# Optimization experiments

Measured on AMD Instinct MI355X. Metric: run time of the kernel, lower is better.

Reference implementation:

```python
import jax, jax.numpy as jnp
import numpy as np

D_MODEL = 1024
D_FF = 4 * D_MODEL
N = D_MODEL * D_FF          # 4,194,304 == 2**22, so pad_n == N (no padding)
PAD_N = N
FFT_LEN = PAD_N // 2 + 1    # 2,097,153 rfft bins
KEEP = int(FFT_LEN * 0.25)  # 524,288 kept coefficients ('medium')
B, S = 4, 2048


def _decompress(cr, ci, idx, shape, scale):
    # scatter top-k complex coeffs into full rfft spectrum, inverse rfft,
    # reshape to weight matrix and rescale (riemann_decompress)
    coeffs = jax.lax.complex(cr, ci)                      # complex64 [KEEP]
    full = jnp.zeros((FFT_LEN,), jnp.complex64).at[idx].set(coeffs)
    w = jnp.fft.irfft(full, n=PAD_N)                      # [PAD_N] real
    return w.reshape(shape) * scale                       # scale is [1], broadcasts


def setup_inputs() -> dict:
    key = jax.random.key(0)
    ks = jax.random.split(key, 9)
    return {
        "x": jax.random.normal(ks[0], (B, S, D_MODEL), jnp.float32),
        "c_fc_coeffs_real": jax.random.normal(ks[1], (KEEP,), jnp.float32),
        "c_fc_coeffs_imag": jax.random.normal(ks[2], (KEEP,), jnp.float32),
        "c_fc_indices": jnp.arange(KEEP, dtype=jnp.int32),
        "c_fc_scale": jax.random.uniform(ks[3], (1,), jnp.float32, 0.5, 1.5),
        "c_fc_bias": jax.random.normal(ks[4], (D_FF,), jnp.float32),
        "c_proj_coeffs_real": jax.random.normal(ks[5], (KEEP,), jnp.float32),
        "c_proj_coeffs_imag": jax.random.normal(ks[6], (KEEP,), jnp.float32),
        "c_proj_indices": jnp.arange(KEEP, dtype=jnp.int32),
        "c_proj_scale": jax.random.uniform(ks[7], (1,), jnp.float32, 0.5, 1.5),
        "c_proj_bias": jax.random.normal(ks[8], (D_MODEL,), jnp.float32),
    }


def reference(x, c_fc_coeffs_real, c_fc_coeffs_imag, c_fc_indices, c_fc_scale,
              c_fc_bias, c_proj_coeffs_real, c_proj_coeffs_imag, c_proj_indices,
              c_proj_scale, c_proj_bias):
    # c_fc.weight stored [d_model, d_ff]; F.linear(x, W.T) == x @ W
    w_fc = _decompress(c_fc_coeffs_real, c_fc_coeffs_imag, c_fc_indices,
                       (D_MODEL, D_FF), c_fc_scale)
    h = jnp.einsum('bsd,df->bsf', x, w_fc) + c_fc_bias
    h = jax.nn.gelu(h, approximate=False)  # nn.GELU() exact erf form
    w_proj = _decompress(c_proj_coeffs_real, c_proj_coeffs_imag, c_proj_indices,
                         (D_FF, D_MODEL), c_proj_scale)
    return jnp.einsum('bsf,fd->bsd', h, w_proj) + c_proj_bias
```

## Files before the change

### kernel.cpp

```cpp
#include <hip/hip_runtime.h>
#include <hip/hip_bf16.h>
#include <hip/hip_fp8.h>
#include <math.h>

#define M_HALF 2097152
#define W_SCALE 256.0f

typedef __bf16 bf16_t;
typedef unsigned char u8;
typedef __attribute__((ext_vector_type(4))) float f32x4;

#define GLOBAL_AS __attribute__((address_space(1)))
#define LDS_AS    __attribute__((address_space(3)))

__device__ __forceinline__ u8 to_fp8(float v) {
    __hip_fp8_e4m3 t(v);
    return *reinterpret_cast<u8*>(&t);
}

__device__ __forceinline__ float2 cadd(float2 a, float2 b){ return make_float2(a.x+b.x, a.y+b.y); }
__device__ __forceinline__ float2 csub(float2 a, float2 b){ return make_float2(a.x-b.x, a.y-b.y); }
__device__ __forceinline__ float2 cmul(float2 a, float2 b){ return make_float2(a.x*b.x-a.y*b.y, a.x*b.y+a.y*b.x); }
__device__ __forceinline__ float2 cmuli(float2 a){ return make_float2(-a.y, a.x); }

__device__ __forceinline__ void radix8_inv(const float2 v[8], float2 X[8]) {
    const float cc = 0.70710678118654752f;
    float2 a0 = cadd(v[0], v[4]), a1 = cadd(v[1], v[5]), a2 = cadd(v[2], v[6]), a3 = cadd(v[3], v[7]);
    float2 b0 = csub(v[0], v[4]), b1 = csub(v[1], v[5]), b2 = csub(v[2], v[6]), b3 = csub(v[3], v[7]);
    b1 = cmul(b1, make_float2(cc, cc));
    b2 = cmuli(b2);
    b3 = cmul(b3, make_float2(-cc, cc));
    float2 c0 = cadd(a0, a2), c1 = cadd(a1, a3), d0 = csub(a0, a2), d1 = cmuli(csub(a1, a3));
    float2 e0 = cadd(b0, b2), e1 = cadd(b1, b3), f0 = csub(b0, b2), f1 = cmuli(csub(b1, b3));
    X[0] = cadd(c0, c1); X[4] = csub(c0, c1); X[2] = cadd(d0, d1); X[6] = csub(d0, d1);
    X[1] = cadd(e0, e1); X[5] = csub(e0, e1); X[3] = cadd(f0, f1); X[7] = csub(f0, f1);
}


__global__ __launch_bounds__(256) void zero2_kernel(float2* p, int n) {
    int i = blockIdx.x*256 + threadIdx.x;
    if (i < n) p[i] = make_float2(0.f, 0.f);
}

__global__ __launch_bounds__(256) void scatter2_kernel(const float* __restrict__ crA,
                                                       const float* __restrict__ ciA,
                                                       const int* __restrict__ idxA,
                                                       const float* __restrict__ crB,
                                                       const float* __restrict__ ciB,
                                                       const int* __restrict__ idxB,
                                                       float2* __restrict__ specA,
                                                       float2* __restrict__ specB, int keep) {
    int i = blockIdx.x*256 + threadIdx.x;
    if (i < keep) {
        int k = idxA[i];
        long pos = (k < M_HALF) ? ((long)(k & 511)*4096 + (k >> 9)) : (long)M_HALF;
        specA[pos] = make_float2(crA[i], ciA[i]);
    } else if (i < 2*keep) {
        int t = i - keep;
        int k = idxB[t];
        long pos = (k < M_HALF) ? ((long)(k & 511)*4096 + (k >> 9)) : (long)M_HALF;
        specB[pos] = make_float2(crB[t], ciB[t]);
    }
}


__global__ __launch_bounds__(512) void ifft_p4096_dual(const float2* __restrict__ specTA,
                                                       const float2* __restrict__ specTB,
                                                       float2* __restrict__ dstA,
                                                       float2* __restrict__ dstB,
                                                       const float* __restrict__ scaleA,
                                                       const float* __restrict__ scaleB) {
    __shared__ float2 L[8*656];
    int bb = blockIdx.x;
    const float2* spec; float2* dst; const float* scale;
    if (bb < 512) { spec = specTA; dst = dstA; scale = scaleA; }
    else          { bb -= 512; spec = specTB; dst = dstB; scale = scaleB; }
    const int j = bb;
    const int x = threadIdx.x;
    const float s = scale[0] * (1.0f/(float)M_HALF);
    float2 v[8];
    {
        float ang0 = (float)(3.14159265358979323846 * (double)(j + 512*x) / 2097152.0);
        float sn, cs; sincosf(ang0, &sn, &cs);
        const float2 step = make_float2(0.98078528040323044913f,
                                        0.19509032201612826785f);
        float2 tw = make_float2(cs, sn);
        const long arow = (long)j * 4096;
        const long brow = (long)(512 - j) * 4096;
#pragma unroll
        for (int u = 0; u < 8; ++u) {
            int t = x + 512*u;
            float2 a = spec[arow + t];
            float2 b;
            if (j == 0) b = (t == 0) ? spec[(long)M_HALF] : spec[4096 - t];
            else        b = spec[brow + 4095 - t];
            if (j == 0 && t == 0) { a.y = 0.0f; b.y = 0.0f; }
            float Er = 0.5f*(a.x + b.x), Ei = 0.5f*(a.y - b.y);
            float Tr = 0.5f*(a.x - b.x), Ti = 0.5f*(a.y + b.y);
            float Or = Tr*tw.x - Ti*tw.y, Oi = Tr*tw.y + Ti*tw.x;
            v[u] = make_float2((Er - Oi)*s, (Ei + Or)*s);
            tw = cmul(tw, step);
        }
    }
    float2 E[8];
    radix8_inv(v, E);
    {
        float cb, sb; sincosf((float)x * 0.0015339807878856412f, &sb, &cb);
        float2 wb = make_float2(cb, sb), w = make_float2(1.f, 0.f);
#pragma unroll
        for (int a = 0; a < 8; ++a) { L[a*656 + x] = cmul(E[a], w); w = cmul(w, wb); }
    }
    __syncthreads();
    const int g = x >> 6, xin = x & 63;
    float2* Lg = L + g*656;
    float2 v2[8];
#pragma unroll
    for (int u2 = 0; u2 < 8; ++u2) v2[u2] = Lg[xin + 64*u2];
    float2 E2[8];
    radix8_inv(v2, E2);
    __syncthreads();
    {
        float cb, sb; sincosf((float)xin * 0.012271846303085130f, &sb, &cb);
        float2 wb = make_float2(cb, sb), w = make_float2(1.f, 0.f);
#pragma unroll
        for (int s8 = 0; s8 < 8; ++s8) { Lg[s8*65 + xin] = cmul(E2[s8], w); w = cmul(w, wb); }
    }
    __syncthreads();
    const int p = xin >> 3, xa = xin & 7;
    float2 g2[8];
#pragma unroll
    for (int xb = 0; xb < 8; ++xb) g2[xb] = Lg[p*65 + xa + 8*xb];
    float2 H2[8];
    radix8_inv(g2, H2);
    __syncthreads();
    {
        float cb, sb; sincosf((float)xa * 0.098174770424681039f, &sb, &cb);
        float2 wb = make_float2(cb, sb), w = make_float2(1.f, 0.f);
#pragma unroll
        for (int o8 = 0; o8 < 8; ++o8) { Lg[p*81 + o8*9 + xa] = cmul(H2[o8], w); w = cmul(w, wb); }
    }
    __syncthreads();
    const int pp = xin & 7, sp = xin >> 3;
    float2 r2[8];
#pragma unroll
    for (int xa2 = 0; xa2 < 8; ++xa2) r2[xa2] = Lg[pp*81 + sp*9 + xa2];
    float2 D[8];
    radix8_inv(r2, D);
    __syncthreads();
#pragma unroll
    for (int ob = 0; ob < 8; ++ob) {
        int sg = g + 8*xin + 512*ob;
        L[sg ^ ((sg >> 4) & 7)] = D[ob];
    }
    __syncthreads();
    const long obase = (long)j * 4096;
#pragma unroll
    for (int e = 0; e < 8; ++e) {
        int idx = x + 512*e;
        dst[obase + idx] = L[idx ^ ((idx >> 4) & 7)];
    }
}


__global__ __launch_bounds__(512) void ifft_p512f8_dual(const float2* __restrict__ srcA,
                                                        u8* __restrict__ dstwA,
                                                        const float2* __restrict__ srcB,
                                                        u8* __restrict__ dstwB) {
    __shared__ float2 ex[8 * 642];
    int bb = blockIdx.x;
    const float2* src; u8* dstw;
    if (bb < 512) { src = srcA; dstw = dstwA; }
    else          { bb -= 512; src = srcB; dstw = dstwB; }
    const int tid = threadIdx.x;
    const int jl = tid & 7, x = tid >> 3;
    const int jg = bb * 8 + jl;
    float2* W = ex + jl * 642;
    float2 v[8];
    {
        float a0 = (float)(6.283185307179586 * (double)jg * (double)x / 2097152.0);
        float sn0, cs0; sincosf(a0, &sn0, &cs0);
        float as = (float)(6.283185307179586 * (double)jg / 32768.0);
        float sns, css; sincosf(as, &sns, &css);
        float2 tw = make_float2(cs0, sn0), stepw = make_float2(css, sns);
#pragma unroll
        for (int u = 0; u < 8; ++u) {
            v[u] = cmul(src[jg + (long)(x + 64*u) * 4096], tw);
            tw = cmul(tw, stepw);
        }
    }
    float2 E[8];
    radix8_inv(v, E);
    {
        float cb, sb; sincosf((float)x * 0.012271846303085130f, &sb, &cb);
        float2 wb = make_float2(cb, sb), w = make_float2(1.f, 0.f);
#pragma unroll
        for (int s8 = 0; s8 < 8; ++s8) {
            W[s8*65 + x] = cmul(E[s8], w);
            w = cmul(w, wb);
        }
    }
    __syncthreads();
    const int p = x >> 3, xa = x & 7;
    float2 g[8];
#pragma unroll
    for (int xb = 0; xb < 8; ++xb) g[xb] = W[p*65 + xa + 8*xb];
    float2 H[8];
    radix8_inv(g, H);
    __syncthreads();
    {
        float cb, sb; sincosf((float)xa * 0.098174770424681039f, &sb, &cb);
        float2 wb = make_float2(cb, sb), w = make_float2(1.f, 0.f);
#pragma unroll
        for (int o8 = 0; o8 < 8; ++o8) {
            W[p*81 + o8*9 + xa] = cmul(H[o8], w);
            w = cmul(w, wb);
        }
    }
    __syncthreads();
    const int pp = x & 7, sp = x >> 3;
    float2 r[8];
#pragma unroll
    for (int xa2 = 0; xa2 < 8; ++xa2) r[xa2] = W[pp*81 + sp*9 + xa2];
    float2 Y[8];
    radix8_inv(r, Y);
#pragma unroll
    for (int ob = 0; ob < 8; ++ob) {
        long n = jg + (long)(x + 64*ob) * 4096;
        unsigned short pk = (unsigned short)to_fp8(Y[ob].x * W_SCALE) |
                            ((unsigned short)to_fp8(Y[ob].y * W_SCALE) << 8);
        ((unsigned short*)dstw)[n] = pk;
    }
}


__global__ __launch_bounds__(256) void transpose_f8_dual(const u8* __restrict__ wA,
                                                         u8* __restrict__ wTA,
                                                         const u8* __restrict__ wB,
                                                         u8* __restrict__ wTB) {
    __shared__ u8 tile[32][36];
    int b = blockIdx.x;
    const u8* w; u8* wT; int R, C, bx, by;
    if (b < 4096) { w = wA; wT = wTA; R = 1024; C = 4096; bx = b & 127; by = b >> 7; }
    else { b -= 4096; w = wB; wT = wTB; R = 4096; C = 1024; bx = b & 31; by = b >> 5; }
    int tx = threadIdx.x & 31, ty = threadIdx.x >> 5;
    long c0 = (long)bx * 32, r0 = (long)by * 32;
#pragma unroll
    for (int i = 0; i < 4; ++i)
        tile[ty + i*8][tx] = w[(r0 + ty + i*8) * C + c0 + tx];
    __syncthreads();
#pragma unroll
    for (int i = 0; i < 4; ++i) {
        int c = ty + i*8;
        wT[(c0 + c) * R + r0 + tx] = tile[tx][c];
    }
}


__global__ __launch_bounds__(256) void cvt_fp8_kernel(const float* __restrict__ in,
                                                      u8* __restrict__ out, int n4) {
    int i = blockIdx.x*256 + threadIdx.x;
    if (i < n4) {
        float4 v = ((const float4*)in)[i];
        unsigned int pk = (unsigned int)to_fp8(v.x) |
                          ((unsigned int)to_fp8(v.y) << 8) |
                          ((unsigned int)to_fp8(v.z) << 16) |
                          ((unsigned int)to_fp8(v.w) << 24);
        ((unsigned int*)out)[i] = pk;
    }
}


template<int NITER>
__device__ __forceinline__ void stage_b(const u8* g, int ldB, int row0, int col0B,
                                        u8* lds, int tid) {
    int w = tid >> 6, l = tid & 63;
    int r8 = l >> 3;
    int cg = ((l & 7) ^ r8) << 4;
#pragma unroll
    for (int i = 0; i < NITER; ++i) {
        int chunk = (i << 3) + w;
        const u8* ga = g + (long)(row0 + chunk*8 + r8) * ldB + col0B + cg;
        u8* la = lds + (chunk << 10);
        __builtin_amdgcn_global_load_lds((const GLOBAL_AS unsigned int*)ga,
                                         (LDS_AS unsigned int*)la, 16, 0, 0);
    }
}


template<int EPI>
__global__ __launch_bounds__(512, 6) void gemm_f8(const u8* __restrict__ A,
                                                  const u8* __restrict__ Bt,
                                                  const float* __restrict__ bias,
                                                  void* __restrict__ Cout,
                                                  int M, int N, int K,
                                                  int CR, int CC, int GXC) {
    __shared__ __align__(16) u8 lA[128*128];
    __shared__ __align__(16) u8 lB[128*128];
    const int tid = threadIdx.x;
    const int l = tid & 63, w = tid >> 6;
    const int wr = w >> 2, wc = w & 3;
    int flat = blockIdx.y * gridDim.x + blockIdx.x;
    int r = flat & 7, q = flat >> 3;
    int ty = (r / GXC) * CR + q / CC;
    int tx = (r % GXC) * CC + q % CC;
    const int row0 = ty * 128, col0 = tx * 128;
    const int lr = l & 15, lq = l >> 4;
    const int xr = (lr & 7) << 4;
    f32x4 acc[4][2] = {};
    for (int k0 = 0; k0 < K; k0 += 128) {
        stage_b<2>(A,  K, row0, k0, lA, tid);
        stage_b<2>(Bt, K, col0, k0, lB, tid);
        __syncthreads();
#pragma unroll
        for (int kk = 0; kk < 4; ++kk) {
            long af[4], bfr[2];
            const int kb = (kk*32 + lq*8) ^ xr;
#pragma unroll
            for (int mi = 0; mi < 4; ++mi)
                af[mi] = *(const long*)(lA + (wr*64 + mi*16 + lr)*128 + kb);
#pragma unroll
            for (int ni = 0; ni < 2; ++ni)
                bfr[ni] = *(const long*)(lB + (wc*32 + ni*16 + lr)*128 + kb);
#pragma unroll
            for (int mi = 0; mi < 4; ++mi)
#pragma unroll
                for (int ni = 0; ni < 2; ++ni)
                    acc[mi][ni] = __builtin_amdgcn_mfma_f32_16x16x32_fp8_fp8(
                        af[mi], bfr[ni], acc[mi][ni], 0, 0, 0);
        }
        __syncthreads();
    }
    const float inv_s = 1.0f / W_SCALE;
#pragma unroll
    for (int mi = 0; mi < 4; ++mi) {
#pragma unroll
        for (int ni = 0; ni < 2; ++ni) {
            int c = col0 + wc*32 + ni*16 + lr;
            float bv = bias[c];
#pragma unroll
            for (int q2 = 0; q2 < 4; ++q2) {
                int rr = row0 + wr*64 + mi*16 + lq*4 + q2;
                float v = acc[mi][ni][q2] * inv_s + bv;
                if constexpr (EPI == 0) {
                    float y = -1.5957691216057308f * (v + 0.044715f * v * v * v);
                    v = v / (1.0f + __expf(y));
                    ((u8*)Cout)[(long)rr * N + c] = to_fp8(v);
                } else {
                    ((float*)Cout)[(long)rr * N + c] = v;
                }
            }
        }
    }
}


extern "C" void kernel_launch(void* const* d_in, const int* in_sizes, int n_in,
                              void* d_out, int out_size, void* d_ws, size_t ws_size,
                              hipStream_t stream) {
    const float* x        = (const float*)d_in[0];
    const float* fc_cr    = (const float*)d_in[1];
    const float* fc_ci    = (const float*)d_in[2];
    const int*   fc_idx   = (const int*)  d_in[3];
    const float* fc_scale = (const float*)d_in[4];
    const float* fc_bias  = (const float*)d_in[5];
    const float* pj_cr    = (const float*)d_in[6];
    const float* pj_ci    = (const float*)d_in[7];
    const int*   pj_idx   = (const int*)  d_in[8];
    const float* pj_scale = (const float*)d_in[9];
    const float* pj_bias  = (const float*)d_in[10];
    const int keep = in_sizes[1];

    char* ws = (char*)d_ws;
    u8* w_fcT = (u8*)(ws + 0);
    u8* w_pjT = (u8*)(ws + 4194304);
    u8* x_f8  = (u8*)(ws + 8388608);
    u8* h_f8  = (u8*)(ws + 16777216);
    const long SP = (long)M_HALF + 64;
    float2* specA = (float2*)(ws + 8388608);
    float2* specB = specA + SP;
    float2* fftA_A = (float2*)(ws + 50331648);
    float2* fftA_B = (float2*)(ws + 67108864);
    u8* w_natA = (u8*)(ws + 8388608);
    u8* w_natB = (u8*)(ws + 12582912);

    zero2_kernel<<<(int)((2*SP + 255)/256), 256, 0, stream>>>(specA, (int)(2*SP));
    scatter2_kernel<<<(2*keep + 255)/256, 256, 0, stream>>>(
        fc_cr, fc_ci, fc_idx, pj_cr, pj_ci, pj_idx, specA, specB, keep);
    ifft_p4096_dual<<<1024, 512, 0, stream>>>(specA, specB, fftA_A, fftA_B,
                                              fc_scale, pj_scale);
    ifft_p512f8_dual<<<1024, 512, 0, stream>>>(fftA_A, w_natA, fftA_B, w_natB);
    transpose_f8_dual<<<8192, 256, 0, stream>>>(w_natA, w_fcT, w_natB, w_pjT);

    cvt_fp8_kernel<<<8388608/4/256, 256, 0, stream>>>(x, x_f8, 8388608/4);

    gemm_f8<0><<<dim3(4096/128, 8192/128), 512, 0, stream>>>(
        x_f8, w_fcT, fc_bias, h_f8, 8192, 4096, 1024, 16, 16, 2);

    gemm_f8<1><<<dim3(1024/128, 8192/128), 512, 0, stream>>>(
        h_f8, w_pjT, pj_bias, d_out, 8192, 1024, 4096, 8, 8, 1);

    (void)n_in; (void)out_size; (void)ws_size;
}
```

Measured before the change: 207.5 us.

## Permute K dimension so GEMM inner loop uses 16-byte LDS fragment loads

Applies a K-index permutation within each 128-wide block to the weights (written by the inverse FFT), to the converted activations, and to the fc GEMM's fp8 output. Because both operands share the same permutation, the dot product is unchanged, and each lane can load 16 bytes at once and issue two MFMAs per load instead of one per 8-byte load. The fp8 conversion kernel is also widened to 8 elements per thread. This halves the number of LDS read instructions, at the cost of extra index arithmetic and scattered stores in the producer kernels.

```diff
diff --git a/kernel.cpp b/kernel.cpp
--- a/kernel.cpp
+++ b/kernel.cpp
@@ -9,6 +9,7 @@
 typedef __bf16 bf16_t;
 typedef unsigned char u8;
 typedef __attribute__((ext_vector_type(4))) float f32x4;
+typedef __attribute__((ext_vector_type(2))) long long2v;
 
 #define GLOBAL_AS __attribute__((address_space(1)))
 #define LDS_AS    __attribute__((address_space(3)))
@@ -16,6 +17,13 @@
 __device__ __forceinline__ u8 to_fp8(float v) {
     __hip_fp8_e4m3 t(v);
     return *reinterpret_cast<u8*>(&t);
+}
+
+__device__ __forceinline__ int perm8(int g) {
+    return (((g >> 3) * 4 + (g & 3)) << 1) + ((g >> 2) & 1);
+}
+__device__ __forceinline__ int permk(int k) {
+    return (k & ~127) | (perm8((k >> 3) & 15) * 8 + (k & 7));
 }
 
 __device__ __forceinline__ float2 cadd(float2 a, float2 b){ return make_float2(a.x+b.x, a.y+b.y); }
@@ -168,9 +176,9 @@
                                                         u8* __restrict__ dstwB) {
     __shared__ float2 ex[8 * 642];
     int bb = blockIdx.x;
-    const float2* src; u8* dstw;
-    if (bb < 512) { src = srcA; dstw = dstwA; }
-    else          { bb -= 512; src = srcB; dstw = dstwB; }
+    const float2* src; u8* dstw; bool isA;
+    if (bb < 512) { src = srcA; dstw = dstwA; isA = true; }
+    else          { bb -= 512; src = srcB; dstw = dstwB; isA = false; }
     const int tid = threadIdx.x;
     const int jl = tid & 7, x = tid >> 3;
     const int jg = bb * 8 + jl;
@@ -225,10 +233,18 @@
     radix8_inv(r, Y);
 #pragma unroll
     for (int ob = 0; ob < 8; ++ob) {
-        long n = jg + (long)(x + 64*ob) * 4096;
+        int sidx = x + 64*ob;
+        long n2;
+        if (isA) {
+            int rr = 2*sidx + (jg >> 11);
+            n2 = (long)permk(rr) * 2048 + (jg & 2047);
+        } else {
+            int rr = 8*sidx + (jg >> 9);
+            n2 = (long)permk(rr) * 512 + (jg & 511);
+        }
         unsigned short pk = (unsigned short)to_fp8(Y[ob].x * W_SCALE) |
                             ((unsigned short)to_fp8(Y[ob].y * W_SCALE) << 8);
-        ((unsigned short*)dstw)[n] = pk;
+        ((unsigned short*)dstw)[n2] = pk;
     }
 }
 
@@ -257,15 +273,20 @@
 
 
 __global__ __launch_bounds__(256) void cvt_fp8_kernel(const float* __restrict__ in,
-                                                      u8* __restrict__ out, int n4) {
+                                                      u8* __restrict__ out, int n8) {
     int i = blockIdx.x*256 + threadIdx.x;
-    if (i < n4) {
-        float4 v = ((const float4*)in)[i];
-        unsigned int pk = (unsigned int)to_fp8(v.x) |
-                          ((unsigned int)to_fp8(v.y) << 8) |
-                          ((unsigned int)to_fp8(v.z) << 16) |
-                          ((unsigned int)to_fp8(v.w) << 24);
-        ((unsigned int*)out)[i] = pk;
+    if (i < n8) {
+        float4 v0 = ((const float4*)in)[i*2];
+        float4 v1 = ((const float4*)in)[i*2+1];
+        unsigned long pk =  (unsigned long)to_fp8(v0.x)
+                         | ((unsigned long)to_fp8(v0.y) << 8)
+                         | ((unsigned long)to_fp8(v0.z) << 16)
+                         | ((unsigned long)to_fp8(v0.w) << 24)
+                         | ((unsigned long)to_fp8(v1.x) << 32)
+                         | ((unsigned long)to_fp8(v1.y) << 40)
+                         | ((unsigned long)to_fp8(v1.z) << 48)
+                         | ((unsigned long)to_fp8(v1.w) << 56);
+        ((unsigned long*)out)[(i >> 4) * 16 + perm8(i & 15)] = pk;
     }
 }
 
@@ -312,21 +333,24 @@
         stage_b<2>(Bt, K, col0, k0, lB, tid);
         __syncthreads();
 #pragma unroll
-        for (int kk = 0; kk < 4; ++kk) {
-            long af[4], bfr[2];
-            const int kb = (kk*32 + lq*8) ^ xr;
+        for (int kk2 = 0; kk2 < 2; ++kk2) {
+            long2v af[4], bfr[2];
+            const int kb = (kk2*64 + lq*16) ^ xr;
 #pragma unroll
             for (int mi = 0; mi < 4; ++mi)
-                af[mi] = *(const long*)(lA + (wr*64 + mi*16 + lr)*128 + kb);
+                af[mi] = *(const long2v*)(lA + (wr*64 + mi*16 + lr)*128 + kb);
 #pragma unroll
             for (int ni = 0; ni < 2; ++ni)
-                bfr[ni] = *(const long*)(lB + (wc*32 + ni*16 + lr)*128 + kb);
+                bfr[ni] = *(const long2v*)(lB + (wc*32 + ni*16 + lr)*128 + kb);
 #pragma unroll
             for (int mi = 0; mi < 4; ++mi)
 #pragma unroll
-                for (int ni = 0; ni < 2; ++ni)
+                for (int ni = 0; ni < 2; ++ni) {
                     acc[mi][ni] = __builtin_amdgcn_mfma_f32_16x16x32_fp8_fp8(
-                        af[mi], bfr[ni], acc[mi][ni], 0, 0, 0);
+                        af[mi][0], bfr[ni][0], acc[mi][ni], 0, 0, 0);
+                    acc[mi][ni] = __builtin_amdgcn_mfma_f32_16x16x32_fp8_fp8(
+                        af[mi][1], bfr[ni][1], acc[mi][ni], 0, 0, 0);
+                }
         }
         __syncthreads();
     }
@@ -344,7 +368,7 @@
                 if constexpr (EPI == 0) {
                     float y = -1.5957691216057308f * (v + 0.044715f * v * v * v);
                     v = v / (1.0f + __expf(y));
-                    ((u8*)Cout)[(long)rr * N + c] = to_fp8(v);
+                    ((u8*)Cout)[(long)rr * N + permk(c)] = to_fp8(v);
                 } else {
                     ((float*)Cout)[(long)rr * N + c] = v;
                 }
@@ -391,7 +415,7 @@
     ifft_p512f8_dual<<<1024, 512, 0, stream>>>(fftA_A, w_natA, fftA_B, w_natB);
     transpose_f8_dual<<<8192, 256, 0, stream>>>(w_natA, w_fcT, w_natB, w_pjT);
 
-    cvt_fp8_kernel<<<8388608/4/256, 256, 0, stream>>>(x, x_f8, 8388608/4);
+    cvt_fp8_kernel<<<8388608/8/256, 256, 0, stream>>>(x, x_f8, 8388608/8);
 
     gemm_f8<0><<<dim3(4096/128, 8192/128), 512, 0, stream>>>(
         x_f8, w_fcT, fc_bias, h_f8, 8192, 4096, 1024, 16, 16, 2);
```

After: 186.6 us. 10.1% less time.
